# Performance work log

Measured on AMD Instinct MI355X. Metric: run time of the kernel, lower is better.

## Reference

```python
import jax, jax.numpy as jnp
import numpy as np

EMBED_DIM = 1024
NUM_HEADS = 16
HEAD_DIM = EMBED_DIM // NUM_HEADS
B, S = 2, 2048


def _xavier(k, shape):
    # xavier_uniform for square [out,in] weight
    limit = float(np.sqrt(6.0 / (shape[0] + shape[1])))
    return jax.random.uniform(k, shape, jnp.float32, -limit, limit)


def setup_inputs() -> dict:
    key = jax.random.key(0)
    ks = jax.random.split(key, 7)
    return {
        "query": jax.random.normal(ks[0], (B, S, EMBED_DIM), jnp.float32),
        "key": jax.random.normal(ks[1], (B, S, EMBED_DIM), jnp.float32),
        "value": jax.random.normal(ks[2], (B, S, EMBED_DIM), jnp.float32),
        "Wq": _xavier(ks[3], (EMBED_DIM, EMBED_DIM)),
        "Wk": _xavier(ks[4], (EMBED_DIM, EMBED_DIM)),
        "Wv": _xavier(ks[5], (EMBED_DIM, EMBED_DIM)),
        "Wo": _xavier(ks[6], (EMBED_DIM, EMBED_DIM)),
    }


def _orthogonalize(Wq, Wk):
    # Both projections computed from the ORIGINAL weights, then both replaced
    # (matches torch: weight1_proj/weight2_proj computed before copy_).
    Wq_o = Wq - Wq @ (Wk.T @ Wk)
    Wk_o = Wk - Wk @ (Wq.T @ Wq)
    return Wq_o, Wk_o


def reference(query, key, value, Wq, Wk, Wv, Wo):
    Wq_o, Wk_o = _orthogonalize(Wq, Wk)
    # F.linear(x, W) = x @ W.T
    q = query @ Wq_o.T
    k = key @ Wk_o.T
    v = value @ Wv.T
    # [B, S, E] -> [B, H, S, Dh]
    def split_heads(x):
        return x.reshape(B, -1, NUM_HEADS, HEAD_DIM).transpose(0, 2, 1, 3)
    q, k, v = split_heads(q), split_heads(k), split_heads(v)
    scale = 1.0 / (HEAD_DIM ** 0.5)
    scores = jnp.einsum("bhqd,bhkd->bhqk", q, k) * scale
    attn = jax.nn.softmax(scores, axis=-1)
    out = jnp.einsum("bhqk,bhkd->bhqd", attn, v)
    out = out.transpose(0, 2, 1, 3).reshape(B, -1, EMBED_DIM)
    return out @ Wo.T
```

## Files before the change

### kernel.cpp

```cpp
#include <hip/hip_runtime.h>
#include <math.h>

constexpr int EMBED  = 1024;
constexpr int NHEADS = 16;
constexpr int HDIM   = 64;
constexpr int BATCH  = 2;
constexpr int SEQ    = 2048;
constexpr int MROWS  = BATCH * SEQ;

typedef unsigned short u16b;
typedef __attribute__((ext_vector_type(8))) short bfrag;
typedef __attribute__((ext_vector_type(4))) float ffrag;
typedef __attribute__((ext_vector_type(16))) float f16frag;
typedef __attribute__((ext_vector_type(4))) int i32x4;

#define SCALE_Q 0.18033688f

__device__ __forceinline__ u16b f2b(float f) {
    union { float f; unsigned u; } v; v.f = f;
    unsigned r = v.u + 0x7fffu + ((v.u >> 16) & 1u);
    return (u16b)(r >> 16);
}

__device__ __forceinline__ unsigned cvtpk_bf16(float a, float b) {
    unsigned r;
    asm("v_cvt_pk_bf16_f32 %0, %1, %2" : "=v"(r) : "v"(a), "v"(b));
    return r;
}

__device__ __forceinline__ void plane_swap(unsigned a, unsigned b, int& lo, int& hi) {
    auto r = __builtin_amdgcn_permlane32_swap((int)a, (int)b, false, false);
    lo = (int)r[0];
    hi = (int)r[1];
}

__device__ __forceinline__ void gload_lds16(const u16b* g, u16b* l) {
    __builtin_amdgcn_global_load_lds(
        (const __attribute__((address_space(1))) void*)g,
        (__attribute__((address_space(3))) void*)l,
        16, 0, 0);
}

template<int N>
__device__ __forceinline__ void wait_vmcnt() {
    if constexpr (N == 0)      asm volatile("s_waitcnt vmcnt(0)" ::: "memory");
    else if constexpr (N == 2) asm volatile("s_waitcnt vmcnt(2)" ::: "memory");
    else if constexpr (N == 3) asm volatile("s_waitcnt vmcnt(3)" ::: "memory");
    else if constexpr (N == 4) asm volatile("s_waitcnt vmcnt(4)" ::: "memory");
    else static_assert(N == 0 || N == 2 || N == 3 || N == 4, "unsupported vmcnt");
}

struct GemmPtrs {
    const u16b* A[3];
    const u16b* B[3];
    const float* D[3];
    u16b* Cb[3];
    float* Cf[3];
    float scale[3];
    int vt[3];
    int hs[3];
};

__global__ void prep_all(const float* __restrict__ q, const float* __restrict__ k,
                         const float* __restrict__ v,
                         const float* __restrict__ Wq, const float* __restrict__ Wk,
                         const float* __restrict__ Wv, const float* __restrict__ Wo,
                         u16b* __restrict__ oq, u16b* __restrict__ ok, u16b* __restrict__ ov,
                         u16b* __restrict__ wq, u16b* __restrict__ wk,
                         u16b* __restrict__ wv, u16b* __restrict__ wo,
                         u16b* __restrict__ wqt, u16b* __restrict__ wkt) {
    const int z = blockIdx.z;
    const int tid = threadIdx.x;
    if (z < 3) {
        const float* src = (z == 0) ? q : (z == 1) ? k : v;
        u16b* dst = (z == 0) ? oq : (z == 1) ? ok : ov;
        const int i = blockIdx.x * 256 + tid;
        float4 val = ((const float4*)src)[i];
        ushort4 o;
        o.x = f2b(val.x); o.y = f2b(val.y); o.z = f2b(val.z); o.w = f2b(val.w);
        ((ushort4*)dst)[i] = o;
        return;
    }
    if (blockIdx.x >= 1024) return;
    const int w = z - 3;
    const float* src = (w == 0) ? Wq : (w == 1) ? Wk : (w == 2) ? Wv : Wo;
    u16b* dst  = (w == 0) ? wq : (w == 1) ? wk : (w == 2) ? wv : wo;
    u16b* dstT = (w == 0) ? wqt : (w == 1) ? wkt : nullptr;
    __shared__ float t[32][33];
    const int bx = (blockIdx.x & 31) * 32, by = (blockIdx.x >> 5) * 32;
    const int x = tid & 31, y = tid >> 5;
#pragma unroll
    for (int r = 0; r < 4; ++r) {
        const int row = by + y + 8 * r;
        const float val = src[(size_t)row * EMBED + bx + x];
        dst[(size_t)row * EMBED + bx + x] = f2b(val);
        if (w < 2) t[y + 8 * r][x] = val;
    }
    if (w >= 2) return;
    __syncthreads();
#pragma unroll
    for (int r = 0; r < 4; ++r)
        dstT[(size_t)(bx + y + 8 * r) * EMBED + by + x] = f2b(t[x][y + 8 * r]);
}

template<int MODE, int BM, int BN>
__global__ __launch_bounds__(256) void gemm_big(GemmPtrs p, int M, int N, int K) {
    const int z = blockIdx.z;
    const u16b* __restrict__ A = p.A[z];
    const u16b* __restrict__ B = p.B[z];
    const float* __restrict__ D = p.D[z];
    u16b* __restrict__ Cb = p.Cb[z];
    float* __restrict__ Cf = p.Cf[z];
    const float scale = p.scale[z];
    const int vt = p.vt[z], hs = p.hs[z];

    constexpr int BK = 32;
    constexpr int IT = BM / 32;
    constexpr int JT = BN / 32;
    constexpr int IA = BM / 64;
    constexpr int IB = BN / 64;
    constexpr int LPW = IA + IB;
    __shared__ __align__(16) u16b As[2][BM * BK];
    __shared__ __align__(16) u16b Bs[2][BN * BK];

    const int tid = threadIdx.x;
    const int wave = tid >> 6, lane = tid & 63;
    const int quad = lane >> 4, l16 = lane & 15;
    const int wrow = wave >> 1, wcol = wave & 1;
    const int m0 = blockIdx.y * BM, n0 = blockIdx.x * BN;

    ffrag acc[IT][JT];
#pragma unroll
    for (int i = 0; i < IT; ++i)
#pragma unroll
        for (int j = 0; j < JT; ++j) acc[i][j] = ffrag{0.f, 0.f, 0.f, 0.f};

    const int srow = lane >> 2, schunk = lane & 3;

    auto STAGE = [&](int buf, int kt) {
#pragma unroll
        for (int q = 0; q < IA; ++q) {
            int row = wave * (BM / 4) + q * 16;
            gload_lds16(A + (size_t)(m0 + row + srow) * K + kt + schunk * 8,
                        &As[buf][row * BK]);
        }
#pragma unroll
        for (int q = 0; q < IB; ++q) {
            int row = wave * (BN / 4) + q * 16;
            gload_lds16(B + (size_t)(n0 + row + srow) * K + kt + schunk * 8,
                        &Bs[buf][row * BK]);
        }
    };

    STAGE(0, 0);
    STAGE(1, BK);
    wait_vmcnt<LPW>();
    __builtin_amdgcn_s_barrier();
    __builtin_amdgcn_sched_barrier(0);

    int cur = 0;
    for (int kt = 0; kt < K; kt += BK, cur ^= 1) {
        bfrag af[IT], bfv[JT];
#pragma unroll
        for (int i = 0; i < IT; ++i)
            af[i] = *(const bfrag*)&As[cur][(wrow * (BM / 2) + i * 16 + l16) * BK + quad * 8];
#pragma unroll
        for (int j = 0; j < JT; ++j)
            bfv[j] = *(const bfrag*)&Bs[cur][(wcol * (BN / 2) + j * 16 + l16) * BK + quad * 8];
        asm volatile("s_waitcnt lgkmcnt(0)" ::: "memory");
        __builtin_amdgcn_sched_barrier(0);
        __builtin_amdgcn_s_barrier();
        __builtin_amdgcn_sched_barrier(0);

        const bool stage = (kt + 2 * BK < K);
        if (stage) STAGE(cur, kt + 2 * BK);

#pragma unroll
        for (int i = 0; i < IT; ++i)
#pragma unroll
            for (int j = 0; j < JT; ++j)
                acc[i][j] = __builtin_amdgcn_mfma_f32_16x16x32_bf16(af[i], bfv[j], acc[i][j], 0, 0, 0);

        if (stage) wait_vmcnt<LPW>();
        else       wait_vmcnt<0>();
        __builtin_amdgcn_s_barrier();
        __builtin_amdgcn_sched_barrier(0);
    }

    if (MODE == 0 && vt) {
#pragma unroll
        for (int i = 0; i < IT; ++i)
#pragma unroll
            for (int j = 0; j < JT; ++j) {
                const int col = n0 + wcol * (BN / 2) + j * 16 + l16;
                const int h = col >> 6, d = col & 63;
                const int row0 = m0 + wrow * (BM / 2) + i * 16 + quad * 4;
                const int b = row0 >> 11, s = row0 & 2047;
                ushort4 o;
                o.x = f2b(acc[i][j][0]); o.y = f2b(acc[i][j][1]);
                o.z = f2b(acc[i][j][2]); o.w = f2b(acc[i][j][3]);
                *(ushort4*)&Cb[((size_t)(b * NHEADS + h) * HDIM + d) * SEQ + s] = o;
            }
        return;
    }
    if (MODE == 0 && hs) {
#pragma unroll
        for (int i = 0; i < IT; ++i)
#pragma unroll
        for (int j = 0; j < JT; ++j) {
                const int col = n0 + wcol * (BN / 2) + j * 16 + l16;
                const int h = col >> 6, d = col & 63;
                const int row0 = m0 + wrow * (BM / 2) + i * 16 + quad * 4;
                const int b = row0 >> 11, s0 = row0 & 2047;
#pragma unroll
                for (int r = 0; r < 4; ++r)
                    Cb[((size_t)(b * NHEADS + h) * SEQ + s0 + r) * HDIM + d] =
                        f2b(acc[i][j][r] * scale);
            }
        return;
    }

#pragma unroll
    for (int i = 0; i < IT; ++i)
#pragma unroll
        for (int j = 0; j < JT; ++j) {
            const int col = n0 + wcol * (BN / 2) + j * 16 + l16;
#pragma unroll
            for (int r = 0; r < 4; ++r) {
                const int row = m0 + wrow * (BM / 2) + i * 16 + quad * 4 + r;
                const size_t idx = (size_t)row * N + col;
                const float v = acc[i][j][r];
                if (MODE == 0) Cb[idx] = f2b(v * scale);
                else if (MODE == 1) Cb[idx] = f2b(D[idx] - v);
                else Cf[idx] = v;
            }
        }
}

__global__ __launch_bounds__(256) void flash_attn6(
    const u16b* __restrict__ Qp, const u16b* __restrict__ Kp,
    const u16b* __restrict__ Vt, float* __restrict__ Opart,
    float* __restrict__ Lpart)
{
    const int tid = threadIdx.x;
    const int wave = tid >> 6, lane = tid & 63;
    const int l32 = lane & 31, hi = lane >> 5;

    const int n = blockIdx.x;
    const int xcd = n & 7, t = n >> 3;
    const int qt = t & 15;
    const int g = ((t >> 4) << 3) | xcd;
    const int h = g >> 2;
    const int b = (g >> 1) & 1, sp = g & 1;

    const int qb = qt * 128 + wave * 32;
    const int kt0 = sp * (SEQ / 2), kt1 = kt0 + SEQ / 2;

    __shared__ __align__(16) u16b Ks[2][64 * 64];
    __shared__ __align__(16) u16b Vs[2][64 * 64];

    const size_t hsbase = (size_t)(b * NHEADS + h) * SEQ;
    const size_t vtbase = (size_t)(b * NHEADS + h) * HDIM * SEQ;
    const size_t obase  = ((size_t)sp * MROWS + (size_t)b * SEQ) * EMBED + h * HDIM;

    bfrag bq[4];
#pragma unroll
    for (int ks = 0; ks < 4; ++ks)
        bq[ks] = *(const bfrag*)&Qp[(hsbase + qb + l32) * HDIM + ks * 16 + hi * 8];

    f16frag ov0, ov1;
#pragma unroll
    for (int r = 0; r < 16; ++r) { ov0[r] = 0.f; ov1[r] = 0.f; }
    float l_run = 0.f;

    const int r0 = tid >> 3, c0 = tid & 7;
    const int sw0 = (r0 * 8 + (c0 ^ (r0 & 7))) * 8;
    const int sw1 = ((r0 + 32) * 8 + (c0 ^ (r0 & 7))) * 8;
    const u16b* kgb = Kp + hsbase * HDIM;
    const u16b* vgb = Vt + vtbase;

    {
        const u16b* kg = kgb + (size_t)kt0 * HDIM;
        bfrag k0 = *(const bfrag*)(kg + tid * 8);
        bfrag k1 = *(const bfrag*)(kg + (tid + 256) * 8);
        bfrag v0 = *(const bfrag*)(vgb + (size_t)r0 * SEQ + kt0 + c0 * 8);
        bfrag v1 = *(const bfrag*)(vgb + (size_t)(r0 + 32) * SEQ + kt0 + c0 * 8);
        *(bfrag*)&Ks[0][sw0] = k0;  *(bfrag*)&Ks[0][sw1] = k1;
        *(bfrag*)&Vs[0][sw0] = v0;  *(bfrag*)&Vs[0][sw1] = v1;
    }
    __syncthreads();

    int p = 0;
    for (int kt = kt0; kt < kt1; kt += 64, p ^= 1) {
        const bool more = (kt + 64) < kt1;
        bfrag kn0, kn1, vn0, vn1;
        if (more) {
            const u16b* kg = kgb + (size_t)(kt + 64) * HDIM;
            kn0 = *(const bfrag*)(kg + tid * 8);
            kn1 = *(const bfrag*)(kg + (tid + 256) * 8);
            vn0 = *(const bfrag*)(vgb + (size_t)r0 * SEQ + kt + 64 + c0 * 8);
            vn1 = *(const bfrag*)(vgb + (size_t)(r0 + 32) * SEQ + kt + 64 + c0 * 8);
        }

        f16frag St0, St1;
#pragma unroll
        for (int r = 0; r < 16; ++r) { St0[r] = 0.f; St1[r] = 0.f; }
#pragma unroll
        for (int ks = 0; ks < 4; ++ks) {
            const int ch = ks * 2 + hi;
            bfrag k0 = *(const bfrag*)&Ks[p][(l32 * 8 + (ch ^ (l32 & 7))) * 8];
            bfrag k1 = *(const bfrag*)&Ks[p][((32 + l32) * 8 + (ch ^ (l32 & 7))) * 8];
            St0 = __builtin_amdgcn_mfma_f32_32x32x16_bf16(k0, bq[ks], St0, 0, 0, 0);
            St1 = __builtin_amdgcn_mfma_f32_32x32x16_bf16(k1, bq[ks], St1, 0, 0, 0);
        }

        float rs = 0.f;
#pragma unroll
        for (int r = 0; r < 16; ++r) {
            const float a = __builtin_amdgcn_exp2f(St0[r]);
            const float c = __builtin_amdgcn_exp2f(St1[r]);
            St0[r] = a; St1[r] = c;
            rs += a + c;
        }
        rs += __shfl_xor(rs, 32);
        l_run += rs;

        unsigned d0[8], d1[8];
#pragma unroll
        for (int rr = 0; rr < 8; ++rr) {
            d0[rr] = cvtpk_bf16(St0[2 * rr], St0[2 * rr + 1]);
            d1[rr] = cvtpk_bf16(St1[2 * rr], St1[2 * rr + 1]);
        }
        bfrag bp[4];
        {
            int a0, a1, b0, b1, c0w, c1, e0, e1;
            plane_swap(d0[0], d0[2], a0, a1);
            plane_swap(d0[1], d0[3], b0, b1);
            i32x4 w = { a0, b0, a1, b1 };
            bp[0] = __builtin_bit_cast(bfrag, w);
            plane_swap(d0[4], d0[6], c0w, c1);
            plane_swap(d0[5], d0[7], e0, e1);
            i32x4 w2 = { c0w, e0, c1, e1 };
            bp[1] = __builtin_bit_cast(bfrag, w2);
        }
        {
            int a0, a1, b0, b1, c0w, c1, e0, e1;
            plane_swap(d1[0], d1[2], a0, a1);
            plane_swap(d1[1], d1[3], b0, b1);
            i32x4 w = { a0, b0, a1, b1 };
            bp[2] = __builtin_bit_cast(bfrag, w);
            plane_swap(d1[4], d1[6], c0w, c1);
            plane_swap(d1[5], d1[7], e0, e1);
            i32x4 w2 = { c0w, e0, c1, e1 };
            bp[3] = __builtin_bit_cast(bfrag, w2);
        }

#pragma unroll
        for (int ks = 0; ks < 4; ++ks) {
            const int ch = ks * 2 + hi;
            bfrag v0 = *(const bfrag*)&Vs[p][(l32 * 8 + (ch ^ (l32 & 7))) * 8];
            bfrag v1 = *(const bfrag*)&Vs[p][((32 + l32) * 8 + (ch ^ (l32 & 7))) * 8];
            ov0 = __builtin_amdgcn_mfma_f32_32x32x16_bf16(v0, bp[ks], ov0, 0, 0, 0);
            ov1 = __builtin_amdgcn_mfma_f32_32x32x16_bf16(v1, bp[ks], ov1, 0, 0, 0);
        }

        if (more) {
            *(bfrag*)&Ks[p ^ 1][sw0] = kn0;  *(bfrag*)&Ks[p ^ 1][sw1] = kn1;
            *(bfrag*)&Vs[p ^ 1][sw0] = vn0;  *(bfrag*)&Vs[p ^ 1][sw1] = vn1;
            __syncthreads();
        }
    }

    const size_t orow = obase + (size_t)(qb + l32) * EMBED;
#pragma unroll
    for (int rr = 0; rr < 4; ++rr) {
        float4 o0, o1;
        o0.x = ov0[4 * rr + 0]; o0.y = ov0[4 * rr + 1];
        o0.z = ov0[4 * rr + 2]; o0.w = ov0[4 * rr + 3];
        o1.x = ov1[4 * rr + 0]; o1.y = ov1[4 * rr + 1];
        o1.z = ov1[4 * rr + 2]; o1.w = ov1[4 * rr + 3];
        *(float4*)&Opart[orow + rr * 8 + hi * 4] = o0;
        *(float4*)&Opart[orow + 32 + rr * 8 + hi * 4] = o1;
    }
    if (hi == 0)
        Lpart[((size_t)sp * BATCH * NHEADS + b * NHEADS + h) * SEQ + qb + l32] = l_run;
}

__global__ void combine_o(const float* __restrict__ O0, const float* __restrict__ O1,
                          const float* __restrict__ L0, const float* __restrict__ L1,
                          u16b* __restrict__ ao) {
    const int i = blockIdx.x * 256 + threadIdx.x;
    const int e0 = i << 2;
    const int row = e0 >> 10, col = e0 & 1023;
    const int lidx = ((row >> 11) * NHEADS + (col >> 6)) * SEQ + (row & 2047);
    float4 a = ((const float4*)O0)[i];
    float4 c = ((const float4*)O1)[i];
    const float inv = 1.f / (L0[lidx] + L1[lidx]);
    ushort4 o;
    o.x = f2b((a.x + c.x) * inv); o.y = f2b((a.y + c.y) * inv);
    o.z = f2b((a.z + c.z) * inv); o.w = f2b((a.w + c.w) * inv);
    ((ushort4*)ao)[i] = o;
}

extern "C" void kernel_launch(void* const* d_in, const int* in_sizes, int n_in,
                              void* d_out, int out_size, void* d_ws, size_t ws_size,
                              hipStream_t stream) {
    const float* query = (const float*)d_in[0];
    const float* key_  = (const float*)d_in[1];
    const float* value = (const float*)d_in[2];
    const float* Wq    = (const float*)d_in[3];
    const float* Wk    = (const float*)d_in[4];
    const float* Wv    = (const float*)d_in[5];
    const float* Wo    = (const float*)d_in[6];
    float* out = (float*)d_out;

    char* ws = (char*)d_ws;
    const size_t MB = 1024 * 1024;
    u16b* xq  = (u16b*)(ws + 0 * MB);
    u16b* xk  = (u16b*)(ws + 8 * MB);
    u16b* xv  = (u16b*)(ws + 16 * MB);
    u16b* wq  = (u16b*)(ws + 24 * MB);
    u16b* wk  = (u16b*)(ws + 26 * MB);
    u16b* wv  = (u16b*)(ws + 28 * MB);
    u16b* gq  = (u16b*)(ws + 32 * MB);
    u16b* gk  = (u16b*)(ws + 34 * MB);
    u16b* wqo = (u16b*)(ws + 36 * MB);
    u16b* wko = (u16b*)(ws + 38 * MB);
    u16b* wo  = (u16b*)(ws + 40 * MB);
    u16b* qp  = (u16b*)(ws + 44 * MB);
    u16b* kp  = (u16b*)(ws + 52 * MB);
    u16b* Vt  = (u16b*)(ws + 60 * MB);
    u16b* wqt = (u16b*)(ws + 60 * MB);
    u16b* wkt = (u16b*)(ws + 62 * MB);
    float* Op  = (float*)(ws + 0 * MB);
    float* Lp  = (float*)(ws + 32 * MB);
    u16b*  ao  = (u16b*)(ws + 44 * MB);

    prep_all<<<dim3(MROWS * EMBED / 1024, 1, 7), dim3(256), 0, stream>>>(
        query, key_, value, Wq, Wk, Wv, Wo,
        xq, xk, xv, wq, wk, wv, wo, wqt, wkt);

    {
        GemmPtrs p{};
        p.A[0] = wqt; p.B[0] = wqt; p.Cb[0] = gq; p.scale[0] = 1.f;
        p.A[1] = wkt; p.B[1] = wkt; p.Cb[1] = gk; p.scale[1] = 1.f;
        gemm_big<0, 64, 64><<<dim3(EMBED / 64, EMBED / 64, 2), dim3(256), 0, stream>>>(
            p, EMBED, EMBED, EMBED);
    }
    {
        GemmPtrs p{};
        p.A[0] = wq; p.B[0] = gk; p.D[0] = Wq; p.Cb[0] = wqo;
        p.A[1] = wk; p.B[1] = gq; p.D[1] = Wk; p.Cb[1] = wko;
        gemm_big<1, 64, 64><<<dim3(EMBED / 64, EMBED / 64, 2), dim3(256), 0, stream>>>(
            p, EMBED, EMBED, EMBED);
    }
    {
        GemmPtrs p{};
        p.A[0] = xq; p.B[0] = wqo; p.Cb[0] = qp; p.scale[0] = SCALE_Q; p.hs[0] = 1;
        p.A[1] = xk; p.B[1] = wko; p.Cb[1] = kp; p.scale[1] = 1.f;     p.hs[1] = 1;
        p.A[2] = xv; p.B[2] = wv;  p.Cb[2] = Vt; p.scale[2] = 1.f;     p.vt[2] = 1;
        gemm_big<0, 128, 128><<<dim3(EMBED / 128, MROWS / 128, 3), dim3(256), 0, stream>>>(
            p, MROWS, EMBED, EMBED);
    }
    flash_attn6<<<dim3(SEQ / 128 * NHEADS * BATCH * 2, 1, 1), dim3(256), 0, stream>>>(
        qp, kp, Vt, Op, Lp);
    combine_o<<<dim3(MROWS * EMBED / 1024), dim3(256), 0, stream>>>(
        Op, Op + (size_t)MROWS * EMBED, Lp, Lp + (size_t)BATCH * NHEADS * SEQ, ao);
    {
        GemmPtrs p{};
        p.A[0] = ao; p.B[0] = wo; p.Cf[0] = out; p.scale[0] = 1.f;
        gemm_big<2, 64, 128><<<dim3(EMBED / 128, MROWS / 64, 1), dim3(256), 0, stream>>>(
            p, MROWS, EMBED, EMBED);
    }
}
```

Measured before the change: 272.6 us.

## Drop split-K attention and fuse normalization into flash attention epilogue

Flash attention no longer splits the key sequence into two halves. Each block now processes the full sequence, divides by the running sum itself and writes bf16 output directly, so the combine kernel is removed. This avoids writing and re-reading fp32 partial outputs and saves one kernel launch. In exchange the grid is halved to 512 blocks with twice the loop length, which may reduce occupancy and load balance across CUs.

```diff
diff --git a/kernel.cpp b/kernel.cpp
--- a/kernel.cpp
+++ b/kernel.cpp
@@ -237,10 +237,9 @@
         }
 }
 
-__global__ __launch_bounds__(256) void flash_attn6(
+__global__ __launch_bounds__(256) void flash_attn8(
     const u16b* __restrict__ Qp, const u16b* __restrict__ Kp,
-    const u16b* __restrict__ Vt, float* __restrict__ Opart,
-    float* __restrict__ Lpart)
+    const u16b* __restrict__ Vt, u16b* __restrict__ ao)
 {
     const int tid = threadIdx.x;
     const int wave = tid >> 6, lane = tid & 63;
@@ -250,18 +249,16 @@
     const int xcd = n & 7, t = n >> 3;
     const int qt = t & 15;
     const int g = ((t >> 4) << 3) | xcd;
-    const int h = g >> 2;
-    const int b = (g >> 1) & 1, sp = g & 1;
+    const int b = g >> 4;
+    const int h = g & 15;
 
     const int qb = qt * 128 + wave * 32;
-    const int kt0 = sp * (SEQ / 2), kt1 = kt0 + SEQ / 2;
 
     __shared__ __align__(16) u16b Ks[2][64 * 64];
     __shared__ __align__(16) u16b Vs[2][64 * 64];
 
     const size_t hsbase = (size_t)(b * NHEADS + h) * SEQ;
     const size_t vtbase = (size_t)(b * NHEADS + h) * HDIM * SEQ;
-    const size_t obase  = ((size_t)sp * MROWS + (size_t)b * SEQ) * EMBED + h * HDIM;
 
     bfrag bq[4];
 #pragma unroll
@@ -280,19 +277,18 @@
     const u16b* vgb = Vt + vtbase;
 
     {
-        const u16b* kg = kgb + (size_t)kt0 * HDIM;
-        bfrag k0 = *(const bfrag*)(kg + tid * 8);
-        bfrag k1 = *(const bfrag*)(kg + (tid + 256) * 8);
-        bfrag v0 = *(const bfrag*)(vgb + (size_t)r0 * SEQ + kt0 + c0 * 8);
-        bfrag v1 = *(const bfrag*)(vgb + (size_t)(r0 + 32) * SEQ + kt0 + c0 * 8);
+        bfrag k0 = *(const bfrag*)(kgb + tid * 8);
+        bfrag k1 = *(const bfrag*)(kgb + (tid + 256) * 8);
+        bfrag v0 = *(const bfrag*)(vgb + (size_t)r0 * SEQ + c0 * 8);
+        bfrag v1 = *(const bfrag*)(vgb + (size_t)(r0 + 32) * SEQ + c0 * 8);
         *(bfrag*)&Ks[0][sw0] = k0;  *(bfrag*)&Ks[0][sw1] = k1;
         *(bfrag*)&Vs[0][sw0] = v0;  *(bfrag*)&Vs[0][sw1] = v1;
     }
     __syncthreads();
 
     int p = 0;
-    for (int kt = kt0; kt < kt1; kt += 64, p ^= 1) {
-        const bool more = (kt + 64) < kt1;
+    for (int kt = 0; kt < SEQ; kt += 64, p ^= 1) {
+        const bool more = (kt + 64) < SEQ;
         bfrag kn0, kn1, vn0, vn1;
         if (more) {
             const u16b* kg = kgb + (size_t)(kt + 64) * HDIM;
@@ -371,35 +367,18 @@
         }
     }
 
-    const size_t orow = obase + (size_t)(qb + l32) * EMBED;
+    const float inv = 1.f / l_run;
+    const size_t orow = ((size_t)b * SEQ + qb + l32) * EMBED + h * HDIM;
 #pragma unroll
     for (int rr = 0; rr < 4; ++rr) {
-        float4 o0, o1;
-        o0.x = ov0[4 * rr + 0]; o0.y = ov0[4 * rr + 1];
-        o0.z = ov0[4 * rr + 2]; o0.w = ov0[4 * rr + 3];
-        o1.x = ov1[4 * rr + 0]; o1.y = ov1[4 * rr + 1];
-        o1.z = ov1[4 * rr + 2]; o1.w = ov1[4 * rr + 3];
-        *(float4*)&Opart[orow + rr * 8 + hi * 4] = o0;
-        *(float4*)&Opart[orow + 32 + rr * 8 + hi * 4] = o1;
-    }
-    if (hi == 0)
-        Lpart[((size_t)sp * BATCH * NHEADS + b * NHEADS + h) * SEQ + qb + l32] = l_run;
-}
-
-__global__ void combine_o(const float* __restrict__ O0, const float* __restrict__ O1,
-                          const float* __restrict__ L0, const float* __restrict__ L1,
-                          u16b* __restrict__ ao) {
-    const int i = blockIdx.x * 256 + threadIdx.x;
-    const int e0 = i << 2;
-    const int row = e0 >> 10, col = e0 & 1023;
-    const int lidx = ((row >> 11) * NHEADS + (col >> 6)) * SEQ + (row & 2047);
-    float4 a = ((const float4*)O0)[i];
-    float4 c = ((const float4*)O1)[i];
-    const float inv = 1.f / (L0[lidx] + L1[lidx]);
-    ushort4 o;
-    o.x = f2b((a.x + c.x) * inv); o.y = f2b((a.y + c.y) * inv);
-    o.z = f2b((a.z + c.z) * inv); o.w = f2b((a.w + c.w) * inv);
-    ((ushort4*)ao)[i] = o;
+        ushort4 o0, o1;
+        o0.x = f2b(ov0[4 * rr + 0] * inv); o0.y = f2b(ov0[4 * rr + 1] * inv);
+        o0.z = f2b(ov0[4 * rr + 2] * inv); o0.w = f2b(ov0[4 * rr + 3] * inv);
+        o1.x = f2b(ov1[4 * rr + 0] * inv); o1.y = f2b(ov1[4 * rr + 1] * inv);
+        o1.z = f2b(ov1[4 * rr + 2] * inv); o1.w = f2b(ov1[4 * rr + 3] * inv);
+        *(ushort4*)&ao[orow + rr * 8 + hi * 4] = o0;
+        *(ushort4*)&ao[orow + 32 + rr * 8 + hi * 4] = o1;
+    }
 }
 
 extern "C" void kernel_launch(void* const* d_in, const int* in_sizes, int n_in,
@@ -432,9 +411,7 @@
     u16b* Vt  = (u16b*)(ws + 60 * MB);
     u16b* wqt = (u16b*)(ws + 60 * MB);
     u16b* wkt = (u16b*)(ws + 62 * MB);
-    float* Op  = (float*)(ws + 0 * MB);
-    float* Lp  = (float*)(ws + 32 * MB);
-    u16b*  ao  = (u16b*)(ws + 44 * MB);
+    u16b* ao  = (u16b*)(ws + 0 * MB);
 
     prep_all<<<dim3(MROWS * EMBED / 1024, 1, 7), dim3(256), 0, stream>>>(
         query, key_, value, Wq, Wk, Wv, Wo,
@@ -462,10 +439,8 @@
         gemm_big<0, 128, 128><<<dim3(EMBED / 128, MROWS / 128, 3), dim3(256), 0, stream>>>(
             p, MROWS, EMBED, EMBED);
     }
-    flash_attn6<<<dim3(SEQ / 128 * NHEADS * BATCH * 2, 1, 1), dim3(256), 0, stream>>>(
-        qp, kp, Vt, Op, Lp);
-    combine_o<<<dim3(MROWS * EMBED / 1024), dim3(256), 0, stream>>>(
-        Op, Op + (size_t)MROWS * EMBED, Lp, Lp + (size_t)BATCH * NHEADS * SEQ, ao);
+    flash_attn8<<<dim3(SEQ / 128 * NHEADS * BATCH, 1, 1), dim3(256), 0, stream>>>(
+        qp, kp, Vt, ao);
     {
         GemmPtrs p{};
         p.A[0] = ao; p.B[0] = wo; p.Cf[0] = out; p.scale[0] = 1.f;
```

After: 259.5 us. 4.8% less time.
